# Performance work log

Measured on AMD Instinct MI355X. Metric: run time of the kernel, lower is better.

Reference implementation:

```python
import jax, jax.numpy as jnp
import numpy as np

B, C, P, H, W = 64, 2048, 4, 14, 14
HID = C * P // 2  # 4096
S = H * W         # 196


def setup_inputs() -> dict:
    key = jax.random.key(0)
    k1, k2, k3, k4, k5 = jax.random.split(key, 5)
    x = jax.random.normal(k1, (B, C, H, W), dtype=jnp.float32)
    w1 = jax.random.normal(k2, (HID, C), dtype=jnp.float32) * 0.02
    b1 = jnp.zeros((HID,), dtype=jnp.float32)
    w2 = jax.random.normal(k3, (C * P, HID), dtype=jnp.float32) * 0.02
    b2 = jnp.zeros((C * P,), dtype=jnp.float32)
    return {"x": x, "w1": w1, "b1": b1, "w2": w2, "b2": b2}


def reference(x, w1, b1, w2, b2):
    # SE-style gating: global average pool -> fc1 -> sigmoid -> fc2 -> sigmoid
    g = x.mean(axis=(2, 3))                                  # [B, C]
    h = jax.nn.sigmoid(g @ w1.T + b1)                        # [B, HID]
    w = jax.nn.sigmoid(h @ w2.T + b2).reshape(B, P, C)       # grouping_result [B, P, C]
    # Weighted feature: mean over channels of w[b,p,c] * x[b,c,s].
    # Original materializes [B,P,C,196] then AdaptiveAvgPool3d over C;
    # mathematically this is a batched matmul divided by C.
    xs = x.reshape(B, C, S)                                  # [B, C, 196]
    feat = jnp.einsum('bpc,bcs->bps', w, xs) / C             # [B, P, 196]
    return (w, feat.reshape(B, P, H, W))
```

## Files before the change

### kernel.cpp

```cpp
#include <hip/hip_runtime.h>
#include <hip/hip_bf16.h>
#include <cstdint>
#include <cstddef>

typedef __attribute__((ext_vector_type(4))) float  f32x4;
typedef __attribute__((ext_vector_type(8))) short  short8;

__device__ __forceinline__ short f2bf(float f) {
  __hip_bfloat16 h = __float2bfloat16(f);
  return *reinterpret_cast<short*>(&h);
}
__device__ __forceinline__ float sigmoidf(float x) {
  return 1.0f / (1.0f + __expf(-x));
}

__global__ __launch_bounds__(256) void pool_kernel(const float* __restrict__ x,
                                                   short* __restrict__ g) {
  __shared__ float sums[784];
  const int tid = threadIdx.x;
  const f32x4* base = (const f32x4*)(x + (size_t)blockIdx.x * (16 * 196));
#pragma unroll
  for (int it = 0; it < 4; ++it) {
    int i = it * 256 + tid;
    if (it < 3 || tid < 16) {
      f32x4 v = base[i];
      sums[i] = v[0] + v[1] + v[2] + v[3];
    }
  }
  __syncthreads();
  if (tid < 16) {
    float s = 0.f;
#pragma unroll
    for (int j = 0; j < 49; ++j) s += sums[tid * 49 + j];
    g[blockIdx.x * 16 + tid] = f2bf(s * (1.0f / 196.0f));
  }
}

template<int N, int K, int WAVES, bool OUT_BF16>
__device__ __forceinline__ void gemm_body(const short* __restrict__ A,
                                          const float* __restrict__ B,
                                          const float* __restrict__ bias,
                                          void* __restrict__ outp,
                                          float* __restrict__ red) {
  constexpr int KW = K / WAVES;
  constexpr int NK = KW / 32;
  constexpr int NT = WAVES * 64;
  const int n0  = blockIdx.x * 16;
  const int tid = threadIdx.x;
  const int l   = tid & 63;
  const int wv  = tid >> 6;
  const int kw0 = wv * KW;

  const int ko = (l >> 4) * 8;
  const float* Bp = B + (size_t)(n0 + (l & 15)) * K + kw0 + ko;
  const short* Ap = A + (size_t)(l & 15) * K + kw0 + ko;

  f32x4 acc0 = {}, acc1 = {}, acc2 = {}, acc3 = {};

  f32x4 bc0 = *(const f32x4*)(Bp);
  f32x4 bc1 = *(const f32x4*)(Bp + 4);
  short8 ac0 = *(const short8*)(Ap);
  short8 ac1 = *(const short8*)(Ap + 16 * K);
  short8 ac2 = *(const short8*)(Ap + 32 * K);
  short8 ac3 = *(const short8*)(Ap + 48 * K);

  for (int t = 0; t < NK; ++t) {
    f32x4 bn0 = {}, bn1 = {};
    short8 an0 = {}, an1 = {}, an2 = {}, an3 = {};
    if (t + 1 < NK) {
      const float* bp = Bp + (t + 1) * 32;
      const short* ap = Ap + (t + 1) * 32;
      bn0 = *(const f32x4*)(bp);
      bn1 = *(const f32x4*)(bp + 4);
      an0 = *(const short8*)(ap);
      an1 = *(const short8*)(ap + 16 * K);
      an2 = *(const short8*)(ap + 32 * K);
      an3 = *(const short8*)(ap + 48 * K);
    }
    short8 bb;
    bb[0] = f2bf(bc0[0]); bb[1] = f2bf(bc0[1]); bb[2] = f2bf(bc0[2]); bb[3] = f2bf(bc0[3]);
    bb[4] = f2bf(bc1[0]); bb[5] = f2bf(bc1[1]); bb[6] = f2bf(bc1[2]); bb[7] = f2bf(bc1[3]);
    acc0 = __builtin_amdgcn_mfma_f32_16x16x32_bf16(ac0, bb, acc0, 0, 0, 0);
    acc1 = __builtin_amdgcn_mfma_f32_16x16x32_bf16(ac1, bb, acc1, 0, 0, 0);
    acc2 = __builtin_amdgcn_mfma_f32_16x16x32_bf16(ac2, bb, acc2, 0, 0, 0);
    acc3 = __builtin_amdgcn_mfma_f32_16x16x32_bf16(ac3, bb, acc3, 0, 0, 0);
    bc0 = bn0; bc1 = bn1;
    ac0 = an0; ac1 = an1; ac2 = an2; ac3 = an3;
  }

  {
    float* rw = red + wv * 1024;
    const int mb = (l >> 4) << 2;
    const int nn = l & 15;
#pragma unroll
    for (int r = 0; r < 4; ++r) rw[(0  + mb + r) * 16 + nn] = acc0[r];
#pragma unroll
    for (int r = 0; r < 4; ++r) rw[(16 + mb + r) * 16 + nn] = acc1[r];
#pragma unroll
    for (int r = 0; r < 4; ++r) rw[(32 + mb + r) * 16 + nn] = acc2[r];
#pragma unroll
    for (int r = 0; r < 4; ++r) rw[(48 + mb + r) * 16 + nn] = acc3[r];
  }
  __syncthreads();

#pragma unroll
  for (int i = tid; i < 1024; i += NT) {
    float s = 0.f;
#pragma unroll
    for (int w = 0; w < WAVES; ++w) s += red[w * 1024 + i];
    int m  = i >> 4;
    int nn = n0 + (i & 15);
    s = sigmoidf(s + bias[nn]);
    if constexpr (OUT_BF16) ((short*)outp)[(size_t)m * N + nn] = f2bf(s);
    else                    ((float*)outp)[(size_t)m * N + nn] = s;
  }
}

__global__ __launch_bounds__(1024, 4) void gemm1_kernel(const short* __restrict__ A,
                                                        const float* __restrict__ B,
                                                        const float* __restrict__ bias,
                                                        short* __restrict__ outp) {
  __shared__ float red[16 * 1024];
  gemm_body<4096, 2048, 16, true>(A, B, bias, outp, red);
}

__global__ __launch_bounds__(512, 4) void gemm2_kernel(const short* __restrict__ A,
                                                       const float* __restrict__ B,
                                                       const float* __restrict__ bias,
                                                       float* __restrict__ outp,
                                                       float* __restrict__ zbuf) {
  constexpr int N = 8192, K = 4096, WAVES = 8, DEPTH = 4;
  constexpr int KW = K / WAVES;
  constexpr int NK = KW / 32;
  __shared__ float red[8 * 1024];

  const int n0  = blockIdx.x * 16;
  const int tid = threadIdx.x;
  const int l   = tid & 63;
  const int wv  = tid >> 6;
  const int kw0 = wv * KW;

  if (tid < 98) zbuf[blockIdx.x * 98 + tid] = 0.f;

  const int ko = (l >> 4) * 8;
  const float* Bp = B + (size_t)(n0 + (l & 15)) * K + kw0 + ko;
  const short* Ap = A + (size_t)(l & 15) * K + kw0 + ko;

  f32x4 acc0 = {}, acc1 = {}, acc2 = {}, acc3 = {};

  f32x4 bq0[DEPTH], bq1[DEPTH];
#pragma unroll
  for (int d = 0; d < DEPTH; ++d) {
    bq0[d] = *(const f32x4*)(Bp + d * 32);
    bq1[d] = *(const f32x4*)(Bp + d * 32 + 4);
  }
  short8 ac0 = *(const short8*)(Ap);
  short8 ac1 = *(const short8*)(Ap + 16 * K);
  short8 ac2 = *(const short8*)(Ap + 32 * K);
  short8 ac3 = *(const short8*)(Ap + 48 * K);

#pragma unroll
  for (int t = 0; t < NK; ++t) {
    const int s = t % DEPTH;
    short8 bb;
    bb[0] = f2bf(bq0[s][0]); bb[1] = f2bf(bq0[s][1]);
    bb[2] = f2bf(bq0[s][2]); bb[3] = f2bf(bq0[s][3]);
    bb[4] = f2bf(bq1[s][0]); bb[5] = f2bf(bq1[s][1]);
    bb[6] = f2bf(bq1[s][2]); bb[7] = f2bf(bq1[s][3]);
    if (t + DEPTH < NK) {
      bq0[s] = *(const f32x4*)(Bp + (t + DEPTH) * 32);
      bq1[s] = *(const f32x4*)(Bp + (t + DEPTH) * 32 + 4);
    }
    if (t + 1 < NK) {
      const short* ap = Ap + (t + 1) * 32;
      short8 an0 = *(const short8*)(ap);
      short8 an1 = *(const short8*)(ap + 16 * K);
      short8 an2 = *(const short8*)(ap + 32 * K);
      short8 an3 = *(const short8*)(ap + 48 * K);
      acc0 = __builtin_amdgcn_mfma_f32_16x16x32_bf16(ac0, bb, acc0, 0, 0, 0);
      acc1 = __builtin_amdgcn_mfma_f32_16x16x32_bf16(ac1, bb, acc1, 0, 0, 0);
      acc2 = __builtin_amdgcn_mfma_f32_16x16x32_bf16(ac2, bb, acc2, 0, 0, 0);
      acc3 = __builtin_amdgcn_mfma_f32_16x16x32_bf16(ac3, bb, acc3, 0, 0, 0);
      ac0 = an0; ac1 = an1; ac2 = an2; ac3 = an3;
    } else {
      acc0 = __builtin_amdgcn_mfma_f32_16x16x32_bf16(ac0, bb, acc0, 0, 0, 0);
      acc1 = __builtin_amdgcn_mfma_f32_16x16x32_bf16(ac1, bb, acc1, 0, 0, 0);
      acc2 = __builtin_amdgcn_mfma_f32_16x16x32_bf16(ac2, bb, acc2, 0, 0, 0);
      acc3 = __builtin_amdgcn_mfma_f32_16x16x32_bf16(ac3, bb, acc3, 0, 0, 0);
    }
  }

  {
    float* rw = red + wv * 1024;
    const int mb = (l >> 4) << 2;
    const int nn = l & 15;
#pragma unroll
    for (int r = 0; r < 4; ++r) rw[(0  + mb + r) * 16 + nn] = acc0[r];
#pragma unroll
    for (int r = 0; r < 4; ++r) rw[(16 + mb + r) * 16 + nn] = acc1[r];
#pragma unroll
    for (int r = 0; r < 4; ++r) rw[(32 + mb + r) * 16 + nn] = acc2[r];
#pragma unroll
    for (int r = 0; r < 4; ++r) rw[(48 + mb + r) * 16 + nn] = acc3[r];
  }
  __syncthreads();
#pragma unroll
  for (int i = tid; i < 1024; i += 512) {
    float s = 0.f;
#pragma unroll
    for (int w = 0; w < 8; ++w) s += red[w * 1024 + i];
    int m  = i >> 4;
    int nn = n0 + (i & 15);
    outp[(size_t)m * N + nn] = sigmoidf(s + bias[nn]);
  }
}

__global__ __launch_bounds__(256) void einsum_kernel(const float* __restrict__ x,
                                                     const float* __restrict__ wg,
                                                     float* __restrict__ feat) {
  const int b   = blockIdx.x >> 4;
  const int cc  = blockIdx.x & 15;
  const int tid = threadIdx.x;
  if (tid >= 196) return;
  const float* wp = wg + (size_t)b * 8192 + cc * 128;
  const float* xp = x + (size_t)b * 2048 * 196 + (size_t)cc * 128 * 196 + tid;
  float a0 = 0.f, a1 = 0.f, a2 = 0.f, a3 = 0.f;
#pragma unroll 8
  for (int c = 0; c < 128; ++c) {
    float xv = xp[(size_t)c * 196];
    a0 = __builtin_fmaf(wp[c],        xv, a0);
    a1 = __builtin_fmaf(wp[2048 + c], xv, a1);
    a2 = __builtin_fmaf(wp[4096 + c], xv, a2);
    a3 = __builtin_fmaf(wp[6144 + c], xv, a3);
  }
  const float invC = 1.0f / 2048.0f;
  atomicAdd(feat + (b * 4 + 0) * 196 + tid, a0 * invC);
  atomicAdd(feat + (b * 4 + 1) * 196 + tid, a1 * invC);
  atomicAdd(feat + (b * 4 + 2) * 196 + tid, a2 * invC);
  atomicAdd(feat + (b * 4 + 3) * 196 + tid, a3 * invC);
}

extern "C" void kernel_launch(void* const* d_in, const int* in_sizes, int n_in,
                              void* d_out, int out_size, void* d_ws, size_t ws_size,
                              hipStream_t stream) {
  const float* x  = (const float*)d_in[0];
  const float* w1 = (const float*)d_in[1];
  const float* b1 = (const float*)d_in[2];
  const float* w2 = (const float*)d_in[3];
  const float* b2 = (const float*)d_in[4];
  float* out = (float*)d_out;

  short* g_bf = (short*)d_ws;
  short* h_bf = g_bf + 64 * 2048;

  float* wout = out;
  float* feat = out + 524288;

  pool_kernel<<<8192, 256, 0, stream>>>(x, g_bf);

  gemm1_kernel<<<4096 / 16, 1024, 0, stream>>>(g_bf, w1, b1, h_bf);

  gemm2_kernel<<<8192 / 16, 512, 0, stream>>>(h_bf, w2, b2, wout, feat);

  einsum_kernel<<<64 * 16, 256, 0, stream>>>(x, wout, feat);
}
```

Baseline: 98.21 us.

## Split gemm2 K dimension across two blocks with separate reduce kernel

```diff
diff --git a/kernel.cpp b/kernel.cpp
--- a/kernel.cpp
+++ b/kernel.cpp
@@ -124,23 +124,18 @@
   gemm_body<4096, 2048, 16, true>(A, B, bias, outp, red);
 }
 
-__global__ __launch_bounds__(512, 4) void gemm2_kernel(const short* __restrict__ A,
-                                                       const float* __restrict__ B,
-                                                       const float* __restrict__ bias,
-                                                       float* __restrict__ outp,
-                                                       float* __restrict__ zbuf) {
-  constexpr int N = 8192, K = 4096, WAVES = 8, DEPTH = 4;
-  constexpr int KW = K / WAVES;
-  constexpr int NK = KW / 32;
+__global__ __launch_bounds__(512, 8) void gemm2_part(const short* __restrict__ A,
+                                                     const float* __restrict__ B,
+                                                     float* __restrict__ part) {
+  constexpr int N = 8192, K = 4096, KW = 256, NK = 8;
   __shared__ float red[8 * 1024];
-
-  const int n0  = blockIdx.x * 16;
+  const int nt = blockIdx.x & 511;
+  const int ks = blockIdx.x >> 9;
+  const int n0 = nt * 16;
   const int tid = threadIdx.x;
   const int l   = tid & 63;
   const int wv  = tid >> 6;
-  const int kw0 = wv * KW;
-
-  if (tid < 98) zbuf[blockIdx.x * 98 + tid] = 0.f;
+  const int kw0 = ks * 2048 + wv * KW;
 
   const int ko = (l >> 4) * 8;
   const float* Bp = B + (size_t)(n0 + (l & 15)) * K + kw0 + ko;
@@ -148,46 +143,35 @@
 
   f32x4 acc0 = {}, acc1 = {}, acc2 = {}, acc3 = {};
 
-  f32x4 bq0[DEPTH], bq1[DEPTH];
-#pragma unroll
-  for (int d = 0; d < DEPTH; ++d) {
-    bq0[d] = *(const f32x4*)(Bp + d * 32);
-    bq1[d] = *(const f32x4*)(Bp + d * 32 + 4);
-  }
+  f32x4 bc0 = *(const f32x4*)(Bp);
+  f32x4 bc1 = *(const f32x4*)(Bp + 4);
   short8 ac0 = *(const short8*)(Ap);
   short8 ac1 = *(const short8*)(Ap + 16 * K);
   short8 ac2 = *(const short8*)(Ap + 32 * K);
   short8 ac3 = *(const short8*)(Ap + 48 * K);
 
-#pragma unroll
   for (int t = 0; t < NK; ++t) {
-    const int s = t % DEPTH;
+    f32x4 bn0 = {}, bn1 = {};
+    short8 an0 = {}, an1 = {}, an2 = {}, an3 = {};
+    if (t + 1 < NK) {
+      const float* bp = Bp + (t + 1) * 32;
+      const short* ap = Ap + (t + 1) * 32;
+      bn0 = *(const f32x4*)(bp);
+      bn1 = *(const f32x4*)(bp + 4);
+      an0 = *(const short8*)(ap);
+      an1 = *(const short8*)(ap + 16 * K);
+      an2 = *(const short8*)(ap + 32 * K);
+      an3 = *(const short8*)(ap + 48 * K);
+    }
     short8 bb;
-    bb[0] = f2bf(bq0[s][0]); bb[1] = f2bf(bq0[s][1]);
-    bb[2] = f2bf(bq0[s][2]); bb[3] = f2bf(bq0[s][3]);
-    bb[4] = f2bf(bq1[s][0]); bb[5] = f2bf(bq1[s][1]);
-    bb[6] = f2bf(bq1[s][2]); bb[7] = f2bf(bq1[s][3]);
-    if (t + DEPTH < NK) {
-      bq0[s] = *(const f32x4*)(Bp + (t + DEPTH) * 32);
-      bq1[s] = *(const f32x4*)(Bp + (t + DEPTH) * 32 + 4);
-    }
-    if (t + 1 < NK) {
-      const short* ap = Ap + (t + 1) * 32;
-      short8 an0 = *(const short8*)(ap);
-      short8 an1 = *(const short8*)(ap + 16 * K);
-      short8 an2 = *(const short8*)(ap + 32 * K);
-      short8 an3 = *(const short8*)(ap + 48 * K);
-      acc0 = __builtin_amdgcn_mfma_f32_16x16x32_bf16(ac0, bb, acc0, 0, 0, 0);
-      acc1 = __builtin_amdgcn_mfma_f32_16x16x32_bf16(ac1, bb, acc1, 0, 0, 0);
-      acc2 = __builtin_amdgcn_mfma_f32_16x16x32_bf16(ac2, bb, acc2, 0, 0, 0);
-      acc3 = __builtin_amdgcn_mfma_f32_16x16x32_bf16(ac3, bb, acc3, 0, 0, 0);
-      ac0 = an0; ac1 = an1; ac2 = an2; ac3 = an3;
-    } else {
-      acc0 = __builtin_amdgcn_mfma_f32_16x16x32_bf16(ac0, bb, acc0, 0, 0, 0);
-      acc1 = __builtin_amdgcn_mfma_f32_16x16x32_bf16(ac1, bb, acc1, 0, 0, 0);
-      acc2 = __builtin_amdgcn_mfma_f32_16x16x32_bf16(ac2, bb, acc2, 0, 0, 0);
-      acc3 = __builtin_amdgcn_mfma_f32_16x16x32_bf16(ac3, bb, acc3, 0, 0, 0);
-    }
+    bb[0] = f2bf(bc0[0]); bb[1] = f2bf(bc0[1]); bb[2] = f2bf(bc0[2]); bb[3] = f2bf(bc0[3]);
+    bb[4] = f2bf(bc1[0]); bb[5] = f2bf(bc1[1]); bb[6] = f2bf(bc1[2]); bb[7] = f2bf(bc1[3]);
+    acc0 = __builtin_amdgcn_mfma_f32_16x16x32_bf16(ac0, bb, acc0, 0, 0, 0);
+    acc1 = __builtin_amdgcn_mfma_f32_16x16x32_bf16(ac1, bb, acc1, 0, 0, 0);
+    acc2 = __builtin_amdgcn_mfma_f32_16x16x32_bf16(ac2, bb, acc2, 0, 0, 0);
+    acc3 = __builtin_amdgcn_mfma_f32_16x16x32_bf16(ac3, bb, acc3, 0, 0, 0);
+    bc0 = bn0; bc1 = bn1;
+    ac0 = an0; ac1 = an1; ac2 = an2; ac3 = an3;
   }
 
   {
@@ -204,15 +188,25 @@
     for (int r = 0; r < 4; ++r) rw[(48 + mb + r) * 16 + nn] = acc3[r];
   }
   __syncthreads();
+
+  float* pp = part + (size_t)ks * (64 * N);
 #pragma unroll
   for (int i = tid; i < 1024; i += 512) {
     float s = 0.f;
 #pragma unroll
     for (int w = 0; w < 8; ++w) s += red[w * 1024 + i];
-    int m  = i >> 4;
-    int nn = n0 + (i & 15);
-    outp[(size_t)m * N + nn] = sigmoidf(s + bias[nn]);
-  }
+    pp[(size_t)(i >> 4) * N + n0 + (i & 15)] = s;
+  }
+}
+
+__global__ __launch_bounds__(512) void gemm2_reduce(const float* __restrict__ part,
+                                                    const float* __restrict__ bias,
+                                                    float* __restrict__ wout,
+                                                    float* __restrict__ feat) {
+  const int i = blockIdx.x * 512 + threadIdx.x;
+  float s = part[i] + part[524288 + i] + bias[i & 8191];
+  wout[i] = sigmoidf(s);
+  if (i < 50176) feat[i] = 0.f;
 }
 
 __global__ __launch_bounds__(256) void einsum_kernel(const float* __restrict__ x,
@@ -252,6 +246,7 @@
 
   short* g_bf = (short*)d_ws;
   short* h_bf = g_bf + 64 * 2048;
+  float* part = (float*)((char*)d_ws + (1 << 20));
 
   float* wout = out;
   float* feat = out + 524288;
@@ -260,7 +255,9 @@
 
   gemm1_kernel<<<4096 / 16, 1024, 0, stream>>>(g_bf, w1, b1, h_bf);
 
-  gemm2_kernel<<<8192 / 16, 512, 0, stream>>>(h_bf, w2, b2, wout, feat);
+  gemm2_part<<<1024, 512, 0, stream>>>(h_bf, w2, part);
+
+  gemm2_reduce<<<1024, 512, 0, stream>>>(part, b2, wout, feat);
 
   einsum_kernel<<<64 * 16, 256, 0, stream>>>(x, wout, feat);
 }
```

Result: slower. 103.9 us (+5.8%).

## Stage gemm2 weight tiles into LDS via async global_load_lds double buffering

Applied to the files above, without the earlier changes.

```diff
diff --git a/kernel.cpp b/kernel.cpp
--- a/kernel.cpp
+++ b/kernel.cpp
@@ -5,6 +5,9 @@
 
 typedef __attribute__((ext_vector_type(4))) float  f32x4;
 typedef __attribute__((ext_vector_type(8))) short  short8;
+
+typedef __attribute__((address_space(3))) uint32_t as3_u32;
+typedef __attribute__((address_space(1))) uint32_t as1_u32;
 
 __device__ __forceinline__ short f2bf(float f) {
   __hip_bfloat16 h = __float2bfloat16(f);
@@ -129,67 +132,82 @@
                                                        const float* __restrict__ bias,
                                                        float* __restrict__ outp,
                                                        float* __restrict__ zbuf) {
-  constexpr int N = 8192, K = 4096, WAVES = 8, DEPTH = 4;
-  constexpr int KW = K / WAVES;
-  constexpr int NK = KW / 32;
-  __shared__ float red[8 * 1024];
-
-  const int n0  = blockIdx.x * 16;
+  constexpr int N = 8192, K = 4096;
+  __shared__ float lds[16384];
   const int tid = threadIdx.x;
   const int l   = tid & 63;
   const int wv  = tid >> 6;
-  const int kw0 = wv * KW;
+  const int n0  = blockIdx.x * 16;
 
   if (tid < 98) zbuf[blockIdx.x * 98 + tid] = 0.f;
 
-  const int ko = (l >> 4) * 8;
-  const float* Bp = B + (size_t)(n0 + (l & 15)) * K + kw0 + ko;
-  const short* Ap = A + (size_t)(l & 15) * K + kw0 + ko;
+  const char*  gB = (const char*)B + (size_t)n0 * (K * 4);
+  const short* Ap = A + (size_t)(l & 15) * K + ((l >> 4) << 3);
 
   f32x4 acc0 = {}, acc1 = {}, acc2 = {}, acc3 = {};
-
-  f32x4 bq0[DEPTH], bq1[DEPTH];
-#pragma unroll
-  for (int d = 0; d < DEPTH; ++d) {
-    bq0[d] = *(const f32x4*)(Bp + d * 32);
-    bq1[d] = *(const f32x4*)(Bp + d * 32 + 4);
-  }
-  short8 ac0 = *(const short8*)(Ap);
-  short8 ac1 = *(const short8*)(Ap + 16 * K);
-  short8 ac2 = *(const short8*)(Ap + 32 * K);
-  short8 ac3 = *(const short8*)(Ap + 48 * K);
-
-#pragma unroll
-  for (int t = 0; t < NK; ++t) {
-    const int s = t % DEPTH;
-    short8 bb;
-    bb[0] = f2bf(bq0[s][0]); bb[1] = f2bf(bq0[s][1]);
-    bb[2] = f2bf(bq0[s][2]); bb[3] = f2bf(bq0[s][3]);
-    bb[4] = f2bf(bq1[s][0]); bb[5] = f2bf(bq1[s][1]);
-    bb[6] = f2bf(bq1[s][2]); bb[7] = f2bf(bq1[s][3]);
-    if (t + DEPTH < NK) {
-      bq0[s] = *(const f32x4*)(Bp + (t + DEPTH) * 32);
-      bq1[s] = *(const f32x4*)(Bp + (t + DEPTH) * 32 + 4);
-    }
-    if (t + 1 < NK) {
-      const short* ap = Ap + (t + 1) * 32;
-      short8 an0 = *(const short8*)(ap);
-      short8 an1 = *(const short8*)(ap + 16 * K);
-      short8 an2 = *(const short8*)(ap + 32 * K);
-      short8 an3 = *(const short8*)(ap + 48 * K);
-      acc0 = __builtin_amdgcn_mfma_f32_16x16x32_bf16(ac0, bb, acc0, 0, 0, 0);
-      acc1 = __builtin_amdgcn_mfma_f32_16x16x32_bf16(ac1, bb, acc1, 0, 0, 0);
-      acc2 = __builtin_amdgcn_mfma_f32_16x16x32_bf16(ac2, bb, acc2, 0, 0, 0);
-      acc3 = __builtin_amdgcn_mfma_f32_16x16x32_bf16(ac3, bb, acc3, 0, 0, 0);
-      ac0 = an0; ac1 = an1; ac2 = an2; ac3 = an3;
-    } else {
-      acc0 = __builtin_amdgcn_mfma_f32_16x16x32_bf16(ac0, bb, acc0, 0, 0, 0);
-      acc1 = __builtin_amdgcn_mfma_f32_16x16x32_bf16(ac1, bb, acc1, 0, 0, 0);
-      acc2 = __builtin_amdgcn_mfma_f32_16x16x32_bf16(ac2, bb, acc2, 0, 0, 0);
-      acc3 = __builtin_amdgcn_mfma_f32_16x16x32_bf16(ac3, bb, acc3, 0, 0, 0);
-    }
-  }
-
+  short8 a_cur[8], a_nxt[8];
+
+#define G2_STAGE(c_, buf_)                                                     \
+  {                                                                            \
+    _Pragma("unroll")                                                          \
+    for (int j = 0; j < 4; ++j) {                                              \
+      int idx = j * 512 + tid;                                                 \
+      int r   = idx >> 7;                                                      \
+      int d   = (idx & 127) << 4;                                              \
+      int s   = d ^ ((r & 7) << 4);                                            \
+      const char* src = gB + (size_t)r * (K * 4) + (size_t)(c_) * 2048 + s;    \
+      char* dst = (char*)lds + (buf_) * 32768 +                                \
+                  (size_t)(j * 512 + (tid & ~63)) * 16;                        \
+      __builtin_amdgcn_global_load_lds((as1_u32*)src, (as3_u32*)dst, 16, 0, 0);\
+    }                                                                          \
+  }
+#define G2_LOADA(c_, ar_)                                                      \
+  {                                                                            \
+    const short* ap = Ap + (c_) * 512 + wv * 64;                               \
+    _Pragma("unroll")                                                          \
+    for (int t = 0; t < 2; ++t) {                                              \
+      _Pragma("unroll")                                                        \
+      for (int f = 0; f < 4; ++f)                                              \
+        ar_[t * 4 + f] = *(const short8*)(ap + t * 32 + (size_t)f * 16 * K);   \
+    }                                                                          \
+  }
+
+  G2_LOADA(0, a_cur);
+  G2_STAGE(0, 0);
+  __syncthreads();
+
+  const int row = l & 15;
+  const int swz = (row & 7) << 4;
+  const int rb  = row * 2048;
+  const int ko4 = ((l >> 4) << 3) << 2;
+
+  for (int c = 0; c < 8; ++c) {
+    if (c < 7) {
+      G2_LOADA(c + 1, a_nxt);
+      G2_STAGE(c + 1, (c + 1) & 1);
+    }
+    const char* bufc = (const char*)lds + (c & 1) * 32768;
+#pragma unroll
+    for (int t = 0; t < 2; ++t) {
+      int kb = (wv << 8) + (t << 7) + ko4;
+      f32x4 b0 = *(const f32x4*)(bufc + rb + ((kb)      ^ swz));
+      f32x4 b1 = *(const f32x4*)(bufc + rb + ((kb + 16) ^ swz));
+      short8 bb;
+      bb[0] = f2bf(b0[0]); bb[1] = f2bf(b0[1]); bb[2] = f2bf(b0[2]); bb[3] = f2bf(b0[3]);
+      bb[4] = f2bf(b1[0]); bb[5] = f2bf(b1[1]); bb[6] = f2bf(b1[2]); bb[7] = f2bf(b1[3]);
+      acc0 = __builtin_amdgcn_mfma_f32_16x16x32_bf16(a_cur[t * 4 + 0], bb, acc0, 0, 0, 0);
+      acc1 = __builtin_amdgcn_mfma_f32_16x16x32_bf16(a_cur[t * 4 + 1], bb, acc1, 0, 0, 0);
+      acc2 = __builtin_amdgcn_mfma_f32_16x16x32_bf16(a_cur[t * 4 + 2], bb, acc2, 0, 0, 0);
+      acc3 = __builtin_amdgcn_mfma_f32_16x16x32_bf16(a_cur[t * 4 + 3], bb, acc3, 0, 0, 0);
+    }
+    __syncthreads();
+    if (c < 7) {
+#pragma unroll
+      for (int i = 0; i < 8; ++i) a_cur[i] = a_nxt[i];
+    }
+  }
+
+  float* red = lds;
   {
     float* rw = red + wv * 1024;
     const int mb = (l >> 4) << 2;
@@ -213,6 +231,8 @@
     int nn = n0 + (i & 15);
     outp[(size_t)m * N + nn] = sigmoidf(s + bias[nn]);
   }
+#undef G2_STAGE
+#undef G2_LOADA
 }
 
 __global__ __launch_bounds__(256) void einsum_kernel(const float* __restrict__ x,
@@ -260,7 +280,7 @@
 
   gemm1_kernel<<<4096 / 16, 1024, 0, stream>>>(g_bf, w1, b1, h_bf);
 
-  gemm2_kernel<<<8192 / 16, 512, 0, stream>>>(h_bf, w2, b2, wout, feat);
+  gemm2_kernel<<<512, 512, 0, stream>>>(h_bf, w2, b2, wout, feat);
 
   einsum_kernel<<<64 * 16, 256, 0, stream>>>(x, wout, feat);
 }
```

New measurement: 96.37 us. No clear change (-1.9%).
